# Kernel tuning notes

Hardware: AMD Instinct MI355X
Metric: run time of the kernel (lower is better)

The kernel has to match this reference:

```python
import jax, jax.numpy as jnp
import numpy as np

B, H, W = 4, 2048, 2048
WEIGHT = 1.0
E_IN = 2.0
E_OUT = 1.0  # unused by the original forward, kept for fidelity
DX = 0.01
DY = 0.01
CONST = 1.0  # constant_value default


def _shift(a, ax, d):
    # edge-replicating shift; d=+1 gives a[i-1], d=-1 gives a[i+1] along axis ax
    if d == 1:
        sl_src = [slice(None)] * a.ndim; sl_edge = [slice(None)] * a.ndim
        sl_src[ax] = slice(None, -1); sl_edge[ax] = slice(None, 1)
    else:
        sl_src = [slice(None)] * a.ndim; sl_edge = [slice(None)] * a.ndim
        sl_src[ax] = slice(1, None); sl_edge[ax] = slice(-1, None)
    if d == 1:
        return jnp.concatenate([a[tuple(sl_edge)], a[tuple(sl_src)]], axis=ax)
    return jnp.concatenate([a[tuple(sl_src)], a[tuple(sl_edge)]], axis=ax)


def compute_gradients(out, mask):
    # out: [B,1,H,W], mask: [H,W] bool -> (grad_x, grad_y) each [B,H,W]
    o = out[:, 0]                      # [B,H,W]
    m_up = _shift(mask, 0, 1);  m_dn = _shift(mask, 0, -1)
    m_lf = _shift(mask, 1, 1);  m_rt = _shift(mask, 1, -1)
    o_up = _shift(o, 1, 1);     o_dn = _shift(o, 1, -1)
    o_lf = _shift(o, 2, 1);     o_rt = _shift(o, 2, -1)
    gx = jnp.where(mask == m_up, (o - o_up) / DX,
                   jnp.where(mask == m_dn, (o - o_dn) / DX, 0.0))
    gy = jnp.where(mask == m_lf, (o - o_lf) / DY,
                   jnp.where(mask == m_rt, (o - o_rt) / DY, 0.0))
    # loops start at i=1, j=1 -> first row and first column stay zero
    valid = (jnp.arange(H)[:, None] >= 1) & (jnp.arange(W)[None, :] >= 1)
    gx = jnp.where(valid, gx, 0.0)
    gy = jnp.where(valid, gy, 0.0)
    return gx, gy


def _masked_mean(sq, bmask):
    # sq: [B,H,W]; mean over batch x selected boundary pixels
    nb = bmask.sum().astype(sq.dtype)
    return jnp.sum(jnp.where(bmask[None], sq, 0.0)) / (sq.shape[0] * nb)


def setup_inputs() -> dict:
    key = jax.random.key(0)
    k1, k2 = jax.random.split(key)
    sub1 = jax.random.normal(k1, (B, 1, H, W), jnp.float32)
    sub2 = jax.random.normal(k2, (B, 1, H, W), jnp.float32)
    yy, xx = np.meshgrid(np.arange(H), np.arange(W), indexing='ij')
    r = np.sqrt((yy - H / 2.0) ** 2 + (xx - W / 2.0) ** 2)
    interface = jnp.asarray(r < H / 4.0)                 # disk subdomain
    boundary = jnp.asarray(np.abs(r - H / 4.0) < 1.0)    # ring at the interface
    return {"subdomain1": sub1, "subdomain2": sub2,
            "interface": interface, "boundary": boundary}


def reference(subdomain1, subdomain2, interface, boundary):
    # masked MSE on the boundary ring
    diff2 = (subdomain1[:, 0] - subdomain2[:, 0]) ** 2      # [B,H,W]
    loss = _masked_mean(diff2, boundary)
    gx1, gy1 = compute_gradients(subdomain1, interface)
    gx2, gy2 = compute_gradients(subdomain2, ~interface)
    loss += _masked_mean((E_IN * gx1 - CONST) ** 2, boundary)
    loss += _masked_mean((E_IN * gy1 - CONST) ** 2, boundary)
    loss += _masked_mean((E_IN * gx2 - CONST) ** 2, boundary)
    loss += _masked_mean((E_IN * gy2 - CONST) ** 2, boundary)
    return loss * WEIGHT
```

## Files before the change

kernel.cpp:

```cpp
#include <hip/hip_runtime.h>
#include <math.h>


#define Ww 2048
#define Bn 4
#define HW (2048 * 2048)
#define NROWS 1025
#define NWAVES (NROWS * 2)
#define BLOCK 256
#define WPB (BLOCK / 64)
#define NBLK ((NWAVES + WPB - 1) / WPB)

__device__ __forceinline__ bool intf(int dy, int dx) {
    return (dy * dy + dx * dx) < 262144;
}

__device__ __forceinline__ double waveReduce(double v) {
#pragma unroll
    for (int off = 32; off > 0; off >>= 1)
        v += __shfl_down(v, off, 64);
    return v;
}

__global__ __launch_bounds__(BLOCK) void stageA(
    const float* __restrict__ s1, const float* __restrict__ s2,
    double* __restrict__ partial)
{
    const int lane = threadIdx.x & 63;
    const int w = blockIdx.x * WPB + (threadIdx.x >> 6);

    double lsum = 0.0, lcnt = 0.0;

    if (w < NWAVES) {
        const int side = w & 1;
        const int dy = (w >> 1) - 512;
        const int dy2 = dy * dy;
        const int a = 263168 - dy2;
        const int b = 261122 - dy2;

        int xhi = (int)sqrt((double)a);
        while ((xhi + 1) * (xhi + 1) <= a) ++xhi;
        while (xhi * xhi > a) --xhi;
        int xlo = 0;
        if (b > 0) {
            xlo = (int)sqrt((double)b);
            while (xlo * xlo < b) ++xlo;
            while (xlo > 0 && (xlo - 1) * (xlo - 1) >= b) --xlo;
        }
        if (side == 1 && xlo < 1) xlo = 1;

        const int x = xlo + lane;
        if (x <= xhi) {
            lcnt = 1.0;
            const int dx = side ? -x : x;
            const int i = 1024 + dy, j = 1024 + dx;

            const bool mc = intf(dy, dx);
            const bool eqx_up = (mc == intf(dy - 1, dx));
            const bool eqx_dn = (mc == intf(dy + 1, dx));
            const bool eqy_lf = (mc == intf(dy, dx - 1));
            const bool eqy_rt = (mc == intf(dy, dx + 1));

            const int base = i * Ww + j;
#pragma unroll
            for (int bb = 0; bb < Bn; ++bb) {
                const float* p1 = s1 + (size_t)bb * HW;
                const float* p2 = s2 + (size_t)bb * HW;
                const float c1 = p1[base];
                const float c2 = p2[base];
                const float d = c1 - c2;
                lsum += (double)(d * d);

                float gx1 = 0.f, gx2 = 0.f, gy1 = 0.f, gy2 = 0.f;
                if (eqx_up) {
                    gx1 = (c1 - p1[base - Ww]) / 0.01f;
                    gx2 = (c2 - p2[base - Ww]) / 0.01f;
                } else if (eqx_dn) {
                    gx1 = (c1 - p1[base + Ww]) / 0.01f;
                    gx2 = (c2 - p2[base + Ww]) / 0.01f;
                }
                if (eqy_lf) {
                    gy1 = (c1 - p1[base - 1]) / 0.01f;
                    gy2 = (c2 - p2[base - 1]) / 0.01f;
                } else if (eqy_rt) {
                    gy1 = (c1 - p1[base + 1]) / 0.01f;
                    gy2 = (c2 - p2[base + 1]) / 0.01f;
                }
                float t;
                t = 2.0f * gx1 - 1.0f; lsum += (double)(t * t);
                t = 2.0f * gy1 - 1.0f; lsum += (double)(t * t);
                t = 2.0f * gx2 - 1.0f; lsum += (double)(t * t);
                t = 2.0f * gy2 - 1.0f; lsum += (double)(t * t);
            }
        }
    }

    const double wsum = waveReduce(lsum);
    const double wcnt = waveReduce(lcnt);
    if (w < NWAVES && lane == 0) {
        partial[2 * w + 0] = wsum;
        partial[2 * w + 1] = wcnt;
    }
}

__global__ __launch_bounds__(BLOCK) void stageB(
    const double* __restrict__ partial, float* __restrict__ out)
{
    double s = 0.0, c = 0.0;
    for (int k = threadIdx.x; k < NWAVES; k += BLOCK) {
        s += partial[2 * k + 0];
        c += partial[2 * k + 1];
    }
    __shared__ double ssum[WPB];
    __shared__ double scnt[WPB];
    s = waveReduce(s);
    c = waveReduce(c);
    const int wave = threadIdx.x >> 6;
    const int lane = threadIdx.x & 63;
    if (lane == 0) { ssum[wave] = s; scnt[wave] = c; }
    __syncthreads();
    if (threadIdx.x == 0) {
        double S = 0.0, C = 0.0;
#pragma unroll
        for (int w = 0; w < WPB; ++w) { S += ssum[w]; C += scnt[w]; }
        out[0] = (float)(S / (4.0 * C));
    }
}

extern "C" void kernel_launch(void* const* d_in, const int* in_sizes, int n_in,
                              void* d_out, int out_size, void* d_ws, size_t ws_size,
                              hipStream_t stream) {
    const float* s1 = (const float*)d_in[0];
    const float* s2 = (const float*)d_in[1];
    double* partial = (double*)d_ws;
    float* out = (float*)d_out;

    stageA<<<NBLK, BLOCK, 0, stream>>>(s1, s2, partial);
    stageB<<<1, BLOCK, 0, stream>>>(partial, out);
}
```

Baseline: 141.9 us.

## Fuse two-stage reduction into one cooperative kernel with grid sync

Folds the per-wave partial sums into a per-block shared-memory reduction, so the partial array shrinks from one entry per wave to one per block. It then launches a single cooperative kernel that uses a grid-wide sync before block 0 does the final reduction, which removes the second kernel launch. If the cooperative launch fails, it falls back to the two-kernel path. The grid barrier and cooperative launch carry their own overhead, and the grid must fit co-resident (about 513 blocks of 256 threads).

```diff
diff --git a/kernel.cpp b/kernel.cpp
--- a/kernel.cpp
+++ b/kernel.cpp
@@ -1,5 +1,8 @@
 #include <hip/hip_runtime.h>
+#include <hip/hip_cooperative_groups.h>
 #include <math.h>
+
+namespace cg = cooperative_groups;
 
 
 #define Ww 2048
@@ -22,84 +25,146 @@
     return v;
 }
 
+__device__ __forceinline__ void annulusWave(
+    int w, int lane, const float* __restrict__ s1, const float* __restrict__ s2,
+    double& lsum, double& lcnt)
+{
+    lsum = 0.0; lcnt = 0.0;
+    if (w >= NWAVES) return;
+
+    const int side = w & 1;
+    const int dy = (w >> 1) - 512;
+    const int dy2 = dy * dy;
+    const int a = 263168 - dy2;
+    const int b = 261122 - dy2;
+
+    int xhi = (int)sqrt((double)a);
+    while ((xhi + 1) * (xhi + 1) <= a) ++xhi;
+    while (xhi * xhi > a) --xhi;
+    int xlo = 0;
+    if (b > 0) {
+        xlo = (int)sqrt((double)b);
+        while (xlo * xlo < b) ++xlo;
+        while (xlo > 0 && (xlo - 1) * (xlo - 1) >= b) --xlo;
+    }
+    if (side == 1 && xlo < 1) xlo = 1;
+
+    const int x = xlo + lane;
+    if (x > xhi) return;
+
+    lcnt = 1.0;
+    const int dx = side ? -x : x;
+    const int i = 1024 + dy, j = 1024 + dx;
+
+    const bool mc = intf(dy, dx);
+    const bool eqx_up = (mc == intf(dy - 1, dx));
+    const bool eqx_dn = (mc == intf(dy + 1, dx));
+    const bool eqy_lf = (mc == intf(dy, dx - 1));
+    const bool eqy_rt = (mc == intf(dy, dx + 1));
+
+    const int base = i * Ww + j;
+#pragma unroll
+    for (int bb = 0; bb < Bn; ++bb) {
+        const float* p1 = s1 + (size_t)bb * HW;
+        const float* p2 = s2 + (size_t)bb * HW;
+        const float c1 = p1[base];
+        const float c2 = p2[base];
+        const float d = c1 - c2;
+        lsum += (double)(d * d);
+
+        float gx1 = 0.f, gx2 = 0.f, gy1 = 0.f, gy2 = 0.f;
+        if (eqx_up) {
+            gx1 = (c1 - p1[base - Ww]) / 0.01f;
+            gx2 = (c2 - p2[base - Ww]) / 0.01f;
+        } else if (eqx_dn) {
+            gx1 = (c1 - p1[base + Ww]) / 0.01f;
+            gx2 = (c2 - p2[base + Ww]) / 0.01f;
+        }
+        if (eqy_lf) {
+            gy1 = (c1 - p1[base - 1]) / 0.01f;
+            gy2 = (c2 - p2[base - 1]) / 0.01f;
+        } else if (eqy_rt) {
+            gy1 = (c1 - p1[base + 1]) / 0.01f;
+            gy2 = (c2 - p2[base + 1]) / 0.01f;
+        }
+        float t;
+        t = 2.0f * gx1 - 1.0f; lsum += (double)(t * t);
+        t = 2.0f * gy1 - 1.0f; lsum += (double)(t * t);
+        t = 2.0f * gx2 - 1.0f; lsum += (double)(t * t);
+        t = 2.0f * gy2 - 1.0f; lsum += (double)(t * t);
+    }
+}
+
+__global__ __launch_bounds__(BLOCK) void fusedCoop(
+    const float* __restrict__ s1, const float* __restrict__ s2,
+    double* __restrict__ partial, float* __restrict__ out)
+{
+    const int lane = threadIdx.x & 63;
+    const int wv = threadIdx.x >> 6;
+    const int w = blockIdx.x * WPB + wv;
+
+    double lsum, lcnt;
+    annulusWave(w, lane, s1, s2, lsum, lcnt);
+
+    __shared__ double ssum[WPB];
+    __shared__ double scnt[WPB];
+
+    const double wsum = waveReduce(lsum);
+    const double wcnt = waveReduce(lcnt);
+    if (lane == 0) { ssum[wv] = wsum; scnt[wv] = wcnt; }
+    __syncthreads();
+    if (threadIdx.x == 0) {
+        double S = 0.0, C = 0.0;
+#pragma unroll
+        for (int k = 0; k < WPB; ++k) { S += ssum[k]; C += scnt[k]; }
+        partial[2 * blockIdx.x + 0] = S;
+        partial[2 * blockIdx.x + 1] = C;
+    }
+
+    cg::this_grid().sync();
+
+    if (blockIdx.x != 0) return;
+
+    double s = 0.0, c = 0.0;
+    for (int k = threadIdx.x; k < NBLK; k += BLOCK) {
+        s += partial[2 * k + 0];
+        c += partial[2 * k + 1];
+    }
+    s = waveReduce(s);
+    c = waveReduce(c);
+    if (lane == 0) { ssum[wv] = s; scnt[wv] = c; }
+    __syncthreads();
+    if (threadIdx.x == 0) {
+        double S = 0.0, C = 0.0;
+#pragma unroll
+        for (int k = 0; k < WPB; ++k) { S += ssum[k]; C += scnt[k]; }
+        out[0] = (float)(S / (4.0 * C));
+    }
+}
+
 __global__ __launch_bounds__(BLOCK) void stageA(
     const float* __restrict__ s1, const float* __restrict__ s2,
     double* __restrict__ partial)
 {
     const int lane = threadIdx.x & 63;
-    const int w = blockIdx.x * WPB + (threadIdx.x >> 6);
-
-    double lsum = 0.0, lcnt = 0.0;
-
-    if (w < NWAVES) {
-        const int side = w & 1;
-        const int dy = (w >> 1) - 512;
-        const int dy2 = dy * dy;
-        const int a = 263168 - dy2;
-        const int b = 261122 - dy2;
-
-        int xhi = (int)sqrt((double)a);
-        while ((xhi + 1) * (xhi + 1) <= a) ++xhi;
-        while (xhi * xhi > a) --xhi;
-        int xlo = 0;
-        if (b > 0) {
-            xlo = (int)sqrt((double)b);
-            while (xlo * xlo < b) ++xlo;
-            while (xlo > 0 && (xlo - 1) * (xlo - 1) >= b) --xlo;
-        }
-        if (side == 1 && xlo < 1) xlo = 1;
-
-        const int x = xlo + lane;
-        if (x <= xhi) {
-            lcnt = 1.0;
-            const int dx = side ? -x : x;
-            const int i = 1024 + dy, j = 1024 + dx;
-
-            const bool mc = intf(dy, dx);
-            const bool eqx_up = (mc == intf(dy - 1, dx));
-            const bool eqx_dn = (mc == intf(dy + 1, dx));
-            const bool eqy_lf = (mc == intf(dy, dx - 1));
-            const bool eqy_rt = (mc == intf(dy, dx + 1));
-
-            const int base = i * Ww + j;
-#pragma unroll
-            for (int bb = 0; bb < Bn; ++bb) {
-                const float* p1 = s1 + (size_t)bb * HW;
-                const float* p2 = s2 + (size_t)bb * HW;
-                const float c1 = p1[base];
-                const float c2 = p2[base];
-                const float d = c1 - c2;
-                lsum += (double)(d * d);
-
-                float gx1 = 0.f, gx2 = 0.f, gy1 = 0.f, gy2 = 0.f;
-                if (eqx_up) {
-                    gx1 = (c1 - p1[base - Ww]) / 0.01f;
-                    gx2 = (c2 - p2[base - Ww]) / 0.01f;
-                } else if (eqx_dn) {
-                    gx1 = (c1 - p1[base + Ww]) / 0.01f;
-                    gx2 = (c2 - p2[base + Ww]) / 0.01f;
-                }
-                if (eqy_lf) {
-                    gy1 = (c1 - p1[base - 1]) / 0.01f;
-                    gy2 = (c2 - p2[base - 1]) / 0.01f;
-                } else if (eqy_rt) {
-                    gy1 = (c1 - p1[base + 1]) / 0.01f;
-                    gy2 = (c2 - p2[base + 1]) / 0.01f;
-                }
-                float t;
-                t = 2.0f * gx1 - 1.0f; lsum += (double)(t * t);
-                t = 2.0f * gy1 - 1.0f; lsum += (double)(t * t);
-                t = 2.0f * gx2 - 1.0f; lsum += (double)(t * t);
-                t = 2.0f * gy2 - 1.0f; lsum += (double)(t * t);
-            }
-        }
-    }
-
+    const int wv = threadIdx.x >> 6;
+    const int w = blockIdx.x * WPB + wv;
+
+    double lsum, lcnt;
+    annulusWave(w, lane, s1, s2, lsum, lcnt);
+
+    __shared__ double ssum[WPB];
+    __shared__ double scnt[WPB];
     const double wsum = waveReduce(lsum);
     const double wcnt = waveReduce(lcnt);
-    if (w < NWAVES && lane == 0) {
-        partial[2 * w + 0] = wsum;
-        partial[2 * w + 1] = wcnt;
+    if (lane == 0) { ssum[wv] = wsum; scnt[wv] = wcnt; }
+    __syncthreads();
+    if (threadIdx.x == 0) {
+        double S = 0.0, C = 0.0;
+#pragma unroll
+        for (int k = 0; k < WPB; ++k) { S += ssum[k]; C += scnt[k]; }
+        partial[2 * blockIdx.x + 0] = S;
+        partial[2 * blockIdx.x + 1] = C;
     }
 }
 
@@ -107,7 +172,7 @@
     const double* __restrict__ partial, float* __restrict__ out)
 {
     double s = 0.0, c = 0.0;
-    for (int k = threadIdx.x; k < NWAVES; k += BLOCK) {
+    for (int k = threadIdx.x; k < NBLK; k += BLOCK) {
         s += partial[2 * k + 0];
         c += partial[2 * k + 1];
     }
@@ -115,14 +180,14 @@
     __shared__ double scnt[WPB];
     s = waveReduce(s);
     c = waveReduce(c);
-    const int wave = threadIdx.x >> 6;
+    const int wv = threadIdx.x >> 6;
     const int lane = threadIdx.x & 63;
-    if (lane == 0) { ssum[wave] = s; scnt[wave] = c; }
-    __syncthreads();
-    if (threadIdx.x == 0) {
-        double S = 0.0, C = 0.0;
-#pragma unroll
-        for (int w = 0; w < WPB; ++w) { S += ssum[w]; C += scnt[w]; }
+    if (lane == 0) { ssum[wv] = s; scnt[wv] = c; }
+    __syncthreads();
+    if (threadIdx.x == 0) {
+        double S = 0.0, C = 0.0;
+#pragma unroll
+        for (int k = 0; k < WPB; ++k) { S += ssum[k]; C += scnt[k]; }
         out[0] = (float)(S / (4.0 * C));
     }
 }
@@ -135,6 +200,12 @@
     double* partial = (double*)d_ws;
     float* out = (float*)d_out;
 
-    stageA<<<NBLK, BLOCK, 0, stream>>>(s1, s2, partial);
-    stageB<<<1, BLOCK, 0, stream>>>(partial, out);
-}
+    void* args[] = { (void*)&s1, (void*)&s2, (void*)&partial, (void*)&out };
+    hipError_t err = hipLaunchCooperativeKernel(
+        (const void*)fusedCoop, dim3(NBLK), dim3(BLOCK), args, 0, stream);
+
+    if (err != hipSuccess) {
+        stageA<<<NBLK, BLOCK, 0, stream>>>(s1, s2, partial);
+        stageB<<<1, BLOCK, 0, stream>>>(partial, out);
+    }
+}
```

After: 197.5 us. +39.2%, slower.
